# Optimization experiments

Measured on AMD Instinct MI355X. Metric: run time of the kernel, lower is better.

The kernel has to match this reference:

```python
import jax, jax.numpy as jnp
import numpy as np

N, CX, CS, H = 2048, 768, 384, 16
D = CX // H  # 48


def _ln(t, eps=1e-5):
    mu = jnp.mean(t, axis=-1, keepdims=True)
    var = jnp.mean(jnp.square(t - mu), axis=-1, keepdims=True)
    return (t - mu) * jax.lax.rsqrt(var + eps)


def setup_inputs() -> dict:
    key = jax.random.key(0)
    ks = jax.random.split(key, 16)
    s = 0.02
    return {
        "x": jax.random.normal(ks[0], (N, CX), jnp.float32),
        "mask": jax.random.randint(ks[1], (N,), 0, 2, jnp.int32),
        "pair_logits": jax.random.normal(ks[2], (H, N, N), jnp.float32),
        "single_cond": jax.random.normal(ks[3], (N, CS), jnp.float32),
        # AdaptiveLayerNorm params (single_cond LN has weight, no bias)
        "ln_sc_w": jnp.ones((CS,), jnp.float32),
        "sc_scale_w": s * jax.random.normal(ks[4], (CS, CX), jnp.float32),
        "sc_scale_b": jnp.zeros((CX,), jnp.float32),
        "sc_bias_w": s * jax.random.normal(ks[5], (CS, CX), jnp.float32),
        # q/k/v/gating projections (stored as (in, out); y = x @ W)
        "q_w": s * jax.random.normal(ks[6], (CX, CX), jnp.float32),
        "q_b": jnp.zeros((CX,), jnp.float32),
        "k_w": s * jax.random.normal(ks[7], (CX, CX), jnp.float32),
        "v_w": s * jax.random.normal(ks[8], (CX, CX), jnp.float32),
        "gate_w": s * jax.random.normal(ks[9], (CX, CX), jnp.float32),
        # AdaLNZero params
        "out_w": s * jax.random.normal(ks[10], (CX, CX), jnp.float32),
        "azc_w": s * jax.random.normal(ks[11], (CS, CX), jnp.float32),
        "azc_b": jnp.zeros((CX,), jnp.float32),
    }


def reference(x, mask, pair_logits, single_cond, ln_sc_w, sc_scale_w, sc_scale_b,
              sc_bias_w, q_w, q_b, k_w, v_w, gate_w, out_w, azc_w, azc_b):
    # AdaptiveLayerNorm (use_single_cond=True)
    xn = _ln(x)                              # (N, CX), no affine
    sc = _ln(single_cond) * ln_sc_w          # (N, CS), weight only
    xa = jax.nn.sigmoid(sc @ sc_scale_w + sc_scale_b) * xn + sc @ sc_bias_w

    # QKV projections, split into heads: (N, H, D)
    q = (xa @ q_w + q_b).reshape(N, H, D)
    k = (xa @ k_w).reshape(N, H, D)
    v = (xa @ v_w).reshape(N, H, D)

    # Attention with per-head additive pair bias and key mask
    logits = jnp.einsum("qhd,khd->hqk", q * (D ** -0.5), k) + pair_logits
    logits = jnp.where(mask.astype(bool)[None, None, :], logits, -1e9)
    w = jax.nn.softmax(logits, axis=-1)      # (H, N, N)
    wa = jnp.einsum("hqk,khd->qhd", w, v).reshape(N, CX)

    # Gating, then AdaLNZero output
    wa = wa * jax.nn.sigmoid(xa @ gate_w)
    out = (wa @ out_w) * jax.nn.sigmoid(sc @ azc_w + azc_b)
    return out
```

## Files before the change

kernel.cpp:

```cpp
#include <hip/hip_runtime.h>
#include <math.h>

#define NN 2048
#define CXX 768
#define CSS 384
#define HH 16
#define DHH 48
#define KSPLIT 2

typedef short bf16x8 __attribute__((ext_vector_type(8)));
typedef float f32x4 __attribute__((ext_vector_type(4)));

#define MFMA16(a,b,c) __builtin_amdgcn_mfma_f32_16x16x32_bf16(a,b,c,0,0,0)

__device__ __forceinline__ unsigned short f2bf(float f){
  unsigned u = __float_as_uint(f);
  u += 0x7FFFu + ((u >> 16) & 1u);
  return (unsigned short)(u >> 16);
}
__device__ __forceinline__ float bf2f(unsigned short u){
  return __uint_as_float(((unsigned)u) << 16);
}
__device__ __forceinline__ void async_copy16(const void* g, void* l){
  __builtin_amdgcn_global_load_lds((const __attribute__((address_space(1))) void*)g,
                                   (__attribute__((address_space(3))) void*)l, 16, 0, 0);
}

__device__ inline float waveReduceSum(float v){
  #pragma unroll
  for(int o=32;o>0;o>>=1) v += __shfl_xor(v,o);
  return v;
}

__global__ __launch_bounds__(256) void transpose_all(
    const float* __restrict__ s0, const float* __restrict__ s1, const float* __restrict__ s2,
    const float* __restrict__ s3, const float* __restrict__ s4, const float* __restrict__ s5,
    const float* __restrict__ s6, const float* __restrict__ s7,
    unsigned short* __restrict__ d_scale, unsigned short* __restrict__ d_bias,
    unsigned short* __restrict__ d_azc, unsigned short* __restrict__ d_qkvg,
    unsigned short* __restrict__ d_out){
  int z = blockIdx.z;
  const float* W; unsigned short* Wt; int K;
  switch(z){
    case 0: W=s0; Wt=d_scale; K=384; break;
    case 1: W=s1; Wt=d_bias;  K=384; break;
    case 2: W=s2; Wt=d_azc;   K=384; break;
    case 3: W=s3; Wt=d_qkvg + 0*589824; K=768; break;
    case 4: W=s4; Wt=d_qkvg + 1*589824; K=768; break;
    case 5: W=s5; Wt=d_qkvg + 2*589824; K=768; break;
    case 6: W=s6; Wt=d_qkvg + 3*589824; K=768; break;
    default: W=s7; Wt=d_out; K=768; break;
  }
  int n0 = blockIdx.x*32, k0 = blockIdx.y*32;
  if(k0 >= K) return;
  __shared__ unsigned short t[32][33];
  int c = threadIdx.x & 31, r = threadIdx.x >> 5;
  #pragma unroll
  for(int i=0;i<32;i+=8){
    float v = W[(size_t)(k0 + r + i)*CXX + n0 + c];
    t[c][r+i] = f2bf(v);
  }
  __syncthreads();
  #pragma unroll
  for(int i=0;i<32;i+=8){
    Wt[(size_t)(n0 + r + i)*K + k0 + c] = t[r+i][c];
  }
}

__global__ __launch_bounds__(384) void ln_fused(const float* __restrict__ x,
    const float* __restrict__ scin, const float* __restrict__ w,
    float* __restrict__ xn, unsigned short* __restrict__ scb){
  int row = blockIdx.x;
  int t = threadIdx.x;
  int wid = t>>6, lane = t&63;
  __shared__ float red[6];
  float a0 = x[(size_t)row*CXX + t];
  float a1 = x[(size_t)row*CXX + 384 + t];
  float s = waveReduceSum(a0+a1);
  if(lane==0) red[wid]=s;
  __syncthreads();
  float mu = (red[0]+red[1]+red[2]+red[3]+red[4]+red[5]) * (1.0f/CXX);
  float d0=a0-mu, d1=a1-mu;
  float q = waveReduceSum(d0*d0+d1*d1);
  __syncthreads();
  if(lane==0) red[wid]=q;
  __syncthreads();
  float var = (red[0]+red[1]+red[2]+red[3]+red[4]+red[5]) * (1.0f/CXX);
  float r = rsqrtf(var + 1e-5f);
  xn[(size_t)row*CXX + t] = d0*r;
  xn[(size_t)row*CXX + 384 + t] = d1*r;
  float b = scin[(size_t)row*CSS + t];
  float s2 = waveReduceSum(b);
  __syncthreads();
  if(lane==0) red[wid]=s2;
  __syncthreads();
  float mu2 = (red[0]+red[1]+red[2]+red[3]+red[4]+red[5]) * (1.0f/CSS);
  float d2 = b - mu2;
  float q2 = waveReduceSum(d2*d2);
  __syncthreads();
  if(lane==0) red[wid]=q2;
  __syncthreads();
  float var2 = (red[0]+red[1]+red[2]+red[3]+red[4]+red[5]) * (1.0f/CSS);
  float r2 = rsqrtf(var2 + 1e-5f);
  scb[(size_t)row*CSS + t] = f2bf(d2*r2*w[t]);
}

__global__ __launch_bounds__(256) void gemm_qkvg(const unsigned short* __restrict__ A,
    const unsigned short* __restrict__ Bt, const float* __restrict__ bias,
    unsigned short* __restrict__ C){
  __shared__ unsigned short As[128*32];
  __shared__ unsigned short Bs[128*32];
  const int tid = threadIdx.x;
  const int w = tid>>6, lane = tid&63;
  const int ln15 = lane&15, hi = lane>>4;
  const int wm = w&1, wn = w>>1;
  const int m0 = blockIdx.y*128, n0 = blockIdx.x*128;
  const int lrow = lane>>2, lk = (lane&3)*8;
  const int K = 768, NC = 3072;

  f32x4 z = {0.f,0.f,0.f,0.f};
  f32x4 acc[4][4];
  #pragma unroll
  for(int i=0;i<4;i++)
    #pragma unroll
    for(int j=0;j<4;j++) acc[i][j] = z;

  for(int k0=0;k0<K;k0+=32){
    const unsigned short* ga = A + (size_t)(m0 + w*32 + lrow)*K + k0 + lk;
    const unsigned short* gb = Bt + (size_t)(n0 + w*32 + lrow)*K + k0 + lk;
    async_copy16(ga,          &As[w*1024]);
    async_copy16(ga + 16*K,   &As[w*1024 + 512]);
    async_copy16(gb,          &Bs[w*1024]);
    async_copy16(gb + 16*K,   &Bs[w*1024 + 512]);
    __syncthreads();
    bf16x8 af[4], bfr[4];
    #pragma unroll
    for(int i=0;i<4;i++) af[i]  = *(const bf16x8*)&As[(wm*64 + i*16 + ln15)*32 + hi*8];
    #pragma unroll
    for(int j=0;j<4;j++) bfr[j] = *(const bf16x8*)&Bs[(wn*64 + j*16 + ln15)*32 + hi*8];
    #pragma unroll
    for(int i=0;i<4;i++)
      #pragma unroll
      for(int j=0;j<4;j++)
        acc[i][j] = MFMA16(af[i], bfr[j], acc[i][j]);
    __syncthreads();
  }

  #pragma unroll
  for(int i=0;i<4;i++)
    #pragma unroll
    for(int j=0;j<4;j++)
      #pragma unroll
      for(int r=0;r<4;r++){
        int gm = m0 + wm*64 + i*16 + hi*4 + r;
        int gn = n0 + wn*64 + j*16 + ln15;
        float v = acc[i][j][r];
        if(gn < 768) v += bias[gn];
        if(gn >= 2304) v = 1.0f/(1.0f + __expf(-v));
        C[(size_t)gm*NC + gn] = f2bf(v);
      }
}

__global__ __launch_bounds__(256) void adaln3(const unsigned short* __restrict__ A,
    const unsigned short* __restrict__ B1, const unsigned short* __restrict__ B2,
    const unsigned short* __restrict__ B3, const float* __restrict__ bs,
    const float* __restrict__ zb, const float* __restrict__ xn,
    unsigned short* __restrict__ xa, float* __restrict__ azc){
  __shared__ unsigned short As[64*32];
  __shared__ unsigned short Bs1[64*32];
  __shared__ unsigned short Bs2[64*32];
  __shared__ unsigned short Bs3[64*32];
  const int tid = threadIdx.x;
  const int w = tid>>6, lane = tid&63;
  const int ln15 = lane&15, hi = lane>>4;
  const int wm = w&1, wn = w>>1;
  const int m0 = blockIdx.y*64, n0 = blockIdx.x*64;
  const int lrow = tid>>2, lk = (tid&3)*8;
  const int K = CSS;

  f32x4 z = {0.f,0.f,0.f,0.f};
  f32x4 acc1[2][2], acc2[2][2], acc3[2][2];
  #pragma unroll
  for(int i=0;i<2;i++)
    #pragma unroll
    for(int j=0;j<2;j++){ acc1[i][j]=z; acc2[i][j]=z; acc3[i][j]=z; }

  for(int k0=0;k0<K;k0+=32){
    async_copy16(A  + (size_t)(m0+lrow)*K + k0 + lk, &As [w*512]);
    async_copy16(B1 + (size_t)(n0+lrow)*K + k0 + lk, &Bs1[w*512]);
    async_copy16(B2 + (size_t)(n0+lrow)*K + k0 + lk, &Bs2[w*512]);
    async_copy16(B3 + (size_t)(n0+lrow)*K + k0 + lk, &Bs3[w*512]);
    __syncthreads();
    bf16x8 af[2], b1f[2], b2f[2], b3f[2];
    #pragma unroll
    for(int i=0;i<2;i++) af[i]  = *(const bf16x8*)&As[(wm*32 + i*16 + ln15)*32 + hi*8];
    #pragma unroll
    for(int j=0;j<2;j++){
      b1f[j] = *(const bf16x8*)&Bs1[(wn*32 + j*16 + ln15)*32 + hi*8];
      b2f[j] = *(const bf16x8*)&Bs2[(wn*32 + j*16 + ln15)*32 + hi*8];
      b3f[j] = *(const bf16x8*)&Bs3[(wn*32 + j*16 + ln15)*32 + hi*8];
    }
    #pragma unroll
    for(int i=0;i<2;i++)
      #pragma unroll
      for(int j=0;j<2;j++){
        acc1[i][j] = MFMA16(af[i], b1f[j], acc1[i][j]);
        acc2[i][j] = MFMA16(af[i], b2f[j], acc2[i][j]);
        acc3[i][j] = MFMA16(af[i], b3f[j], acc3[i][j]);
      }
    __syncthreads();
  }

  #pragma unroll
  for(int i=0;i<2;i++)
    #pragma unroll
    for(int j=0;j<2;j++)
      #pragma unroll
      for(int r=0;r<4;r++){
        int gm = m0 + wm*32 + i*16 + hi*4 + r;
        int gn = n0 + wn*32 + j*16 + ln15;
        float g = 1.0f/(1.0f + __expf(-(acc1[i][j][r] + bs[gn])));
        float v = g * xn[(size_t)gm*CXX + gn] + acc2[i][j][r];
        xa[(size_t)gm*CXX + gn] = f2bf(v);
        azc[(size_t)gm*CXX + gn] = 1.0f/(1.0f + __expf(-(acc3[i][j][r] + zb[gn])));
      }
}

__global__ __launch_bounds__(256) void gemm_out(const unsigned short* __restrict__ A,
    const unsigned short* __restrict__ Bt, const float* __restrict__ mul,
    float* __restrict__ C){
  __shared__ unsigned short As[64*32];
  __shared__ unsigned short Bs[64*32];
  const int tid = threadIdx.x;
  const int w = tid>>6, lane = tid&63;
  const int ln15 = lane&15, hi = lane>>4;
  const int wm = w&1, wn = w>>1;
  const int m0 = blockIdx.y*64, n0 = blockIdx.x*64;
  const int lrow = tid>>2, lk = (tid&3)*8;
  const int K = 768;

  f32x4 z = {0.f,0.f,0.f,0.f};
  f32x4 acc[2][2];
  #pragma unroll
  for(int i=0;i<2;i++)
    #pragma unroll
    for(int j=0;j<2;j++) acc[i][j]=z;

  for(int k0=0;k0<K;k0+=32){
    async_copy16(A  + (size_t)(m0+lrow)*K + k0 + lk, &As[w*512]);
    async_copy16(Bt + (size_t)(n0+lrow)*K + k0 + lk, &Bs[w*512]);
    __syncthreads();
    bf16x8 af[2], bfr[2];
    #pragma unroll
    for(int i=0;i<2;i++) af[i]  = *(const bf16x8*)&As[(wm*32 + i*16 + ln15)*32 + hi*8];
    #pragma unroll
    for(int j=0;j<2;j++) bfr[j] = *(const bf16x8*)&Bs[(wn*32 + j*16 + ln15)*32 + hi*8];
    #pragma unroll
    for(int i=0;i<2;i++)
      #pragma unroll
      for(int j=0;j<2;j++)
        acc[i][j] = MFMA16(af[i], bfr[j], acc[i][j]);
    __syncthreads();
  }

  #pragma unroll
  for(int i=0;i<2;i++)
    #pragma unroll
    for(int j=0;j<2;j++)
      #pragma unroll
      for(int r=0;r<4;r++){
        int gm = m0 + wm*32 + i*16 + hi*4 + r;
        int gn = n0 + wn*32 + j*16 + ln15;
        C[(size_t)gm*CXX + gn] = acc[i][j][r] * mul[(size_t)gm*CXX + gn];
      }
}

__global__ __launch_bounds__(256) void attn_mfma(const unsigned short* __restrict__ qkvg,
    const float* __restrict__ pair, const int* __restrict__ mask,
    float* __restrict__ po, float* __restrict__ pm, float* __restrict__ pl){
  const int h = blockIdx.y;
  const int q0 = blockIdx.x*64;
  const int kz = blockIdx.z;
  const int kbase = kz*(NN/KSPLIT);
  const int NT = (NN/KSPLIT)/64;
  const int tid = threadIdx.x;
  const int w = tid>>6, lane = tid&63;
  const int ln15 = lane&15, hi = lane>>4;

  __shared__ unsigned short QPs[64*72];
  __shared__ unsigned short Ks[64*72];
  __shared__ unsigned short VsT[48*72];

  for(int idx=tid; idx<64*16; idx+=256){
    int row = idx>>4, d = 48 + (idx&15);
    QPs[row*72 + d] = 0;
    Ks[row*72 + d] = 0;
  }
  for(int idx=tid; idx<64*12; idx+=256){
    int qr = idx&63, d0 = (idx>>6)*4;
    ushort4 v = *(const ushort4*)&qkvg[(size_t)(q0+qr)*3072 + h*DHH + d0];
    *(ushort4*)&QPs[qr*72 + d0] = v;
  }
  __syncthreads();

  bf16x8 aq0 = *(const bf16x8*)&QPs[(w*16+ln15)*72 + hi*8];
  bf16x8 aq1 = *(const bf16x8*)&QPs[(w*16+ln15)*72 + 32 + hi*8];
  unsigned short* Ps = &QPs[w*16*72];

  f32x4 z = {0.f,0.f,0.f,0.f};
  f32x4 oacc[3] = {z,z,z};
  float mold[4] = {-1e30f,-1e30f,-1e30f,-1e30f};
  float l[4] = {0.f,0.f,0.f,0.f};
  const float scale = 0.14433756729740643f;
  const int qrb = w*16 + hi*4;

  ushort4 kreg[3], vreg[3];
  int mreg[4];
  float preg[4][4];
  {
    #pragma unroll
    for(int it=0;it<3;it++){
      int idx = tid + it*256;
      int key = idx&63, d0 = (idx>>6)*4;
      kreg[it] = *(const ushort4*)&qkvg[(size_t)(kbase+key)*3072 +  768 + h*DHH + d0];
      vreg[it] = *(const ushort4*)&qkvg[(size_t)(kbase+key)*3072 + 1536 + h*DHH + d0];
    }
    #pragma unroll
    for(int jt=0;jt<4;jt++) mreg[jt] = mask[kbase + jt*16 + ln15];
    const float* pb = pair + ((size_t)h*NN + (size_t)(q0+qrb))*NN + kbase + ln15;
    #pragma unroll
    for(int r=0;r<4;r++)
      #pragma unroll
      for(int jt=0;jt<4;jt++)
        preg[jt][r] = pb[(size_t)r*NN + jt*16];
  }

  for(int kt=0; kt<NT; ++kt){
    __syncthreads();
    #pragma unroll
    for(int it=0;it<3;it++){
      int idx = tid + it*256;
      int key = idx&63, d0 = (idx>>6)*4;
      ushort4 kv = kreg[it];
      *(ushort4*)&Ks[key*72 + d0] = kv;
      ushort4 vv = vreg[it];
      VsT[(d0+0)*72 + key] = vv.x;
      VsT[(d0+1)*72 + key] = vv.y;
      VsT[(d0+2)*72 + key] = vv.z;
      VsT[(d0+3)*72 + key] = vv.w;
    }
    __syncthreads();

    float pc[4][4]; int mc[4];
    #pragma unroll
    for(int jt=0;jt<4;jt++){
      mc[jt] = mreg[jt];
      #pragma unroll
      for(int r=0;r<4;r++) pc[jt][r] = preg[jt][r];
    }
    {
      int k0n = (kt < NT-1) ? kbase + (kt+1)*64 : kbase;
      #pragma unroll
      for(int it=0;it<3;it++){
        int idx = tid + it*256;
        int key = idx&63, d0 = (idx>>6)*4;
        kreg[it] = *(const ushort4*)&qkvg[(size_t)(k0n+key)*3072 +  768 + h*DHH + d0];
        vreg[it] = *(const ushort4*)&qkvg[(size_t)(k0n+key)*3072 + 1536 + h*DHH + d0];
      }
      #pragma unroll
      for(int jt=0;jt<4;jt++) mreg[jt] = mask[k0n + jt*16 + ln15];
      const float* pb = pair + ((size_t)h*NN + (size_t)(q0+qrb))*NN + k0n + ln15;
      #pragma unroll
      for(int r=0;r<4;r++)
        #pragma unroll
        for(int jt=0;jt<4;jt++)
          preg[jt][r] = pb[(size_t)r*NN + jt*16];
    }

    f32x4 sreg[4];
    __builtin_amdgcn_s_setprio(1);
    #pragma unroll
    for(int jt=0;jt<4;jt++){
      bf16x8 bk0 = *(const bf16x8*)&Ks[(jt*16+ln15)*72 + hi*8];
      bf16x8 bk1 = *(const bf16x8*)&Ks[(jt*16+ln15)*72 + 32 + hi*8];
      f32x4 s = z;
      s = MFMA16(aq0, bk0, s);
      s = MFMA16(aq1, bk1, s);
      sreg[jt] = s;
    }
    __builtin_amdgcn_s_setprio(0);

    float sv[4][4];
    #pragma unroll
    for(int jt=0;jt<4;jt++)
      #pragma unroll
      for(int r=0;r<4;r++)
        sv[jt][r] = mc[jt] ? sreg[jt][r]*scale + pc[jt][r] : -1e9f;

    float mr[4], al[4], rs[4];
    #pragma unroll
    for(int r=0;r<4;r++)
      mr[r] = fmaxf(fmaxf(sv[0][r],sv[1][r]), fmaxf(sv[2][r],sv[3][r]));
    #pragma unroll
    for(int o=1;o<16;o<<=1)
      #pragma unroll
      for(int r=0;r<4;r++) mr[r] = fmaxf(mr[r], __shfl_xor(mr[r],o));
    #pragma unroll
    for(int r=0;r<4;r++){
      float mn = fmaxf(mold[r], mr[r]);
      al[r] = __expf(mold[r] - mn);
      mold[r] = mn;
    }
    float pv[4][4];
    #pragma unroll
    for(int jt=0;jt<4;jt++)
      #pragma unroll
      for(int r=0;r<4;r++)
        pv[jt][r] = __expf(sv[jt][r] - mold[r]);
    #pragma unroll
    for(int r=0;r<4;r++) rs[r] = pv[0][r]+pv[1][r]+pv[2][r]+pv[3][r];
    #pragma unroll
    for(int o=1;o<16;o<<=1)
      #pragma unroll
      for(int r=0;r<4;r++) rs[r] += __shfl_xor(rs[r],o);
    #pragma unroll
    for(int r=0;r<4;r++) l[r] = l[r]*al[r] + rs[r];

    #pragma unroll
    for(int jt=0;jt<4;jt++)
      #pragma unroll
      for(int r=0;r<4;r++)
        Ps[(hi*4+r)*72 + jt*16 + ln15] = f2bf(pv[jt][r]);
    __asm__ volatile("s_waitcnt lgkmcnt(0)" ::: "memory");

    #pragma unroll
    for(int dt=0;dt<3;dt++)
      #pragma unroll
      for(int r=0;r<4;r++) oacc[dt][r] *= al[r];

    bf16x8 ap0 = *(const bf16x8*)&Ps[ln15*72 + hi*8];
    bf16x8 ap1 = *(const bf16x8*)&Ps[ln15*72 + 32 + hi*8];
    __builtin_amdgcn_s_setprio(1);
    #pragma unroll
    for(int dt=0;dt<3;dt++){
      bf16x8 bv0 = *(const bf16x8*)&VsT[(dt*16+ln15)*72 + hi*8];
      bf16x8 bv1 = *(const bf16x8*)&VsT[(dt*16+ln15)*72 + 32 + hi*8];
      oacc[dt] = MFMA16(ap0, bv0, oacc[dt]);
      oacc[dt] = MFMA16(ap1, bv1, oacc[dt]);
    }
    __builtin_amdgcn_s_setprio(0);
  }

  #pragma unroll
  for(int r=0;r<4;r++){
    int qrow = q0 + qrb + r;
    size_t rowi = (size_t)(kz*HH + h)*NN + qrow;
    #pragma unroll
    for(int dt=0;dt<3;dt++)
      po[rowi*DHH + dt*16 + ln15] = oacc[dt][r];
    if(ln15==0){
      pm[rowi] = mold[r];
      pl[rowi] = l[r];
    }
  }
}

__global__ __launch_bounds__(256) void attn_combine(const float* __restrict__ po,
    const float* __restrict__ pm, const float* __restrict__ pl,
    const unsigned short* __restrict__ qkvg, unsigned short* __restrict__ wag){
  const int row = blockIdx.x*4 + (threadIdx.x>>6);
  const int lane = threadIdx.x & 63;
  #pragma unroll
  for(int i=0;i<12;i++){
    int c = lane + i*64;
    int hh = c / DHH, d = c - hh*DHH;
    size_t r0 = (size_t)hh*NN + row;
    size_t r1 = (size_t)(HH + hh)*NN + row;
    float m0 = pm[r0], m1 = pm[r1];
    float M = fmaxf(m0, m1);
    float e0 = __expf(m0 - M), e1 = __expf(m1 - M);
    float L = pl[r0]*e0 + pl[r1]*e1;
    float v = (po[r0*DHH + d]*e0 + po[r1*DHH + d]*e1) / L;
    float g = bf2f(qkvg[(size_t)row*3072 + 2304 + c]);
    wag[(size_t)row*CXX + c] = f2bf(v * g);
  }
}

extern "C" void kernel_launch(void* const* d_in, const int* in_sizes, int n_in,
                              void* d_out, int out_size, void* d_ws, size_t ws_size,
                              hipStream_t stream) {
  const float* x           = (const float*)d_in[0];
  const int*   mask        = (const int*)  d_in[1];
  const float* pair        = (const float*)d_in[2];
  const float* single_cond = (const float*)d_in[3];
  const float* ln_sc_w     = (const float*)d_in[4];
  const float* sc_scale_w  = (const float*)d_in[5];
  const float* sc_scale_b  = (const float*)d_in[6];
  const float* sc_bias_w   = (const float*)d_in[7];
  const float* q_w         = (const float*)d_in[8];
  const float* q_b         = (const float*)d_in[9];
  const float* k_w         = (const float*)d_in[10];
  const float* v_w         = (const float*)d_in[11];
  const float* gate_w      = (const float*)d_in[12];
  const float* out_w       = (const float*)d_in[13];
  const float* azc_w       = (const float*)d_in[14];
  const float* azc_b       = (const float*)d_in[15];
  float* out = (float*)d_out;

  unsigned short* p = (unsigned short*)d_ws;
  unsigned short* Wt_scale = p;  p += 768*384;
  unsigned short* Wt_bias  = p;  p += 768*384;
  unsigned short* Wt_azc   = p;  p += 768*384;
  unsigned short* Wt_out   = p;  p += 768*768;
  unsigned short* Wt_qkvg  = p;  p += (size_t)3072*768;
  unsigned short* scb      = p;  p += 2048*384;
  unsigned short* xa       = p;  p += 2048*768;
  unsigned short* qkvg     = p;  p += (size_t)2048*3072;
  unsigned short* wag      = p;  p += 2048*768;
  float* fp = (float*)p;
  float* xn  = fp; fp += (size_t)2048*768;
  float* azc = fp; fp += (size_t)2048*768;
  float* po  = fp; fp += (size_t)KSPLIT*HH*NN*DHH;
  float* pm  = fp; fp += (size_t)KSPLIT*HH*NN;
  float* pl  = fp;

  transpose_all<<<dim3(24,24,8), 256, 0, stream>>>(
      sc_scale_w, sc_bias_w, azc_w, q_w, k_w, v_w, gate_w, out_w,
      Wt_scale, Wt_bias, Wt_azc, Wt_qkvg, Wt_out);

  ln_fused<<<NN, 384, 0, stream>>>(x, single_cond, ln_sc_w, xn, scb);

  adaln3<<<dim3(12,32), 256, 0, stream>>>(scb, Wt_scale, Wt_bias, Wt_azc,
                                          sc_scale_b, azc_b, xn, xa, azc);

  gemm_qkvg<<<dim3(24,16), 256, 0, stream>>>(xa, Wt_qkvg, q_b, qkvg);

  attn_mfma<<<dim3(32,16,KSPLIT), 256, 0, stream>>>(qkvg, pair, mask, po, pm, pl);

  attn_combine<<<512, 256, 0, stream>>>(po, pm, pl, qkvg, wag);

  gemm_out<<<dim3(12,32), 256, 0, stream>>>(wag, Wt_out, azc, out);
}
```

Measured before the change: 556.7 us.

## Load attention K/V fragments straight from global with a transposed V buffer

The QKV GEMM epilogue now writes V transposed into a separate buffer (head-dim major), so V fragments can be read in MFMA operand layout. The attention kernel drops LDS staging of Q, K and V and their block-wide barriers. Each wave loads its K and V fragments directly from global memory into registers, double-buffered across an unroll-by-two tile loop. This removes LDS transposes and __syncthreads per tile. In exchange the four waves redundantly fetch the same K/V through cache, and register pressure rises.

```diff
diff --git a/kernel.cpp b/kernel.cpp
--- a/kernel.cpp
+++ b/kernel.cpp
@@ -107,7 +107,7 @@
 
 __global__ __launch_bounds__(256) void gemm_qkvg(const unsigned short* __restrict__ A,
     const unsigned short* __restrict__ Bt, const float* __restrict__ bias,
-    unsigned short* __restrict__ C){
+    unsigned short* __restrict__ C, unsigned short* __restrict__ vt){
   __shared__ unsigned short As[128*32];
   __shared__ unsigned short Bs[128*32];
   const int tid = threadIdx.x;
@@ -149,16 +149,26 @@
   #pragma unroll
   for(int i=0;i<4;i++)
     #pragma unroll
-    for(int j=0;j<4;j++)
-      #pragma unroll
-      for(int r=0;r<4;r++){
-        int gm = m0 + wm*64 + i*16 + hi*4 + r;
-        int gn = n0 + wn*64 + j*16 + ln15;
-        float v = acc[i][j][r];
-        if(gn < 768) v += bias[gn];
-        if(gn >= 2304) v = 1.0f/(1.0f + __expf(-v));
-        C[(size_t)gm*NC + gn] = f2bf(v);
+    for(int j=0;j<4;j++){
+      int gm0 = m0 + wm*64 + i*16 + hi*4;
+      int gn  = n0 + wn*64 + j*16 + ln15;
+      if(gn >= 1536 && gn < 2304){
+        ushort4 v4;
+        v4.x = f2bf(acc[i][j][0]);
+        v4.y = f2bf(acc[i][j][1]);
+        v4.z = f2bf(acc[i][j][2]);
+        v4.w = f2bf(acc[i][j][3]);
+        *(ushort4*)&vt[(size_t)(gn - 1536)*NN + gm0] = v4;
+      } else {
+        #pragma unroll
+        for(int r=0;r<4;r++){
+          float v = acc[i][j][r];
+          if(gn < 768) v += bias[gn];
+          if(gn >= 2304) v = 1.0f/(1.0f + __expf(-v));
+          C[(size_t)(gm0+r)*NC + gn] = f2bf(v);
+        }
       }
+    }
 }
 
 __global__ __launch_bounds__(256) void adaln3(const unsigned short* __restrict__ A,
@@ -275,9 +285,103 @@
       }
 }
 
+
+#define LOAD_TILE(B, KOFF) do{                                                     \
+    int kk_ = (KOFF);                                                              \
+    _Pragma("unroll")                                                              \
+    for(int jt=0;jt<4;jt++){                                                       \
+      const unsigned short* kp_ = qkvg + (size_t)(kk_ + jt*16 + ln15)*3072 + 768 + h*DHH + hi*8; \
+      kf0[B][jt] = *(const bf16x8*)kp_;                                            \
+      kf1[B][jt] = *(const bf16x8*)(kp_ + 32);                                     \
+    }                                                                              \
+    _Pragma("unroll")                                                              \
+    for(int jt=0;jt<4;jt++) mkr[B][jt] = mask[kk_ + jt*16 + ln15];                 \
+    const float* pb_ = pair + ((size_t)h*NN + (size_t)(q0+qrb))*NN + kk_ + ln15;   \
+    _Pragma("unroll")                                                              \
+    for(int r=0;r<4;r++)                                                           \
+      _Pragma("unroll")                                                            \
+      for(int jt=0;jt<4;jt++)                                                      \
+        pfr[B][jt][r] = pb_[(size_t)r*NN + jt*16];                                 \
+  }while(0)
+
+#define ATTN_TILE(B, NB, KCUR, KNXT) do{                                           \
+    bf16x8 vf0[3], vf1[3];                                                         \
+    _Pragma("unroll")                                                              \
+    for(int dt=0;dt<3;dt++){                                                       \
+      const unsigned short* vp_ = vt + (size_t)(h*DHH + dt*16 + ln15)*NN + (KCUR) + hi*8; \
+      vf0[dt] = *(const bf16x8*)vp_;                                               \
+      vf1[dt] = *(const bf16x8*)(vp_ + 32);                                        \
+    }                                                                              \
+    f32x4 sreg[4];                                                                 \
+    __builtin_amdgcn_s_setprio(1);                                                 \
+    _Pragma("unroll")                                                              \
+    for(int jt=0;jt<4;jt++){                                                       \
+      f32x4 s_ = z;                                                                \
+      s_ = MFMA16(aq0, kf0[B][jt], s_);                                            \
+      s_ = MFMA16(aq1, kf1[B][jt], s_);                                            \
+      sreg[jt] = s_;                                                               \
+    }                                                                              \
+    __builtin_amdgcn_s_setprio(0);                                                 \
+    LOAD_TILE(NB, KNXT);                                                           \
+    float sv[4][4];                                                                \
+    _Pragma("unroll")                                                              \
+    for(int jt=0;jt<4;jt++)                                                        \
+      _Pragma("unroll")                                                            \
+      for(int r=0;r<4;r++)                                                         \
+        sv[jt][r] = mkr[B][jt] ? sreg[jt][r]*scale + pfr[B][jt][r] : -1e9f;        \
+    float mrow[4], al[4], rs[4];                                                   \
+    _Pragma("unroll")                                                              \
+    for(int r=0;r<4;r++)                                                           \
+      mrow[r] = fmaxf(fmaxf(sv[0][r],sv[1][r]), fmaxf(sv[2][r],sv[3][r]));         \
+    _Pragma("unroll")                                                              \
+    for(int o=1;o<16;o<<=1)                                                        \
+      _Pragma("unroll")                                                            \
+      for(int r=0;r<4;r++) mrow[r] = fmaxf(mrow[r], __shfl_xor(mrow[r],o));        \
+    _Pragma("unroll")                                                              \
+    for(int r=0;r<4;r++){                                                          \
+      float mn_ = fmaxf(mold[r], mrow[r]);                                         \
+      al[r] = __expf(mold[r] - mn_);                                               \
+      mold[r] = mn_;                                                               \
+    }                                                                              \
+    float pv[4][4];                                                                \
+    _Pragma("unroll")                                                              \
+    for(int jt=0;jt<4;jt++)                                                        \
+      _Pragma("unroll")                                                            \
+      for(int r=0;r<4;r++)                                                         \
+        pv[jt][r] = __expf(sv[jt][r] - mold[r]);                                   \
+    _Pragma("unroll")                                                              \
+    for(int r=0;r<4;r++) rs[r] = pv[0][r]+pv[1][r]+pv[2][r]+pv[3][r];              \
+    _Pragma("unroll")                                                              \
+    for(int o=1;o<16;o<<=1)                                                        \
+      _Pragma("unroll")                                                            \
+      for(int r=0;r<4;r++) rs[r] += __shfl_xor(rs[r],o);                           \
+    _Pragma("unroll")                                                              \
+    for(int r=0;r<4;r++) l[r] = l[r]*al[r] + rs[r];                                \
+    _Pragma("unroll")                                                              \
+    for(int jt=0;jt<4;jt++)                                                        \
+      _Pragma("unroll")                                                            \
+      for(int r=0;r<4;r++)                                                         \
+        Ps[w][(hi*4+r)*72 + jt*16 + ln15] = f2bf(pv[jt][r]);                       \
+    __asm__ volatile("s_waitcnt lgkmcnt(0)" ::: "memory");                         \
+    _Pragma("unroll")                                                              \
+    for(int dt=0;dt<3;dt++)                                                        \
+      _Pragma("unroll")                                                            \
+      for(int r=0;r<4;r++) oacc[dt][r] *= al[r];                                   \
+    bf16x8 ap0 = *(const bf16x8*)&Ps[w][ln15*72 + hi*8];                           \
+    bf16x8 ap1 = *(const bf16x8*)&Ps[w][ln15*72 + 32 + hi*8];                      \
+    __builtin_amdgcn_s_setprio(1);                                                 \
+    _Pragma("unroll")                                                              \
+    for(int dt=0;dt<3;dt++){                                                       \
+      oacc[dt] = MFMA16(ap0, vf0[dt], oacc[dt]);                                   \
+      oacc[dt] = MFMA16(ap1, vf1[dt], oacc[dt]);                                   \
+    }                                                                              \
+    __builtin_amdgcn_s_setprio(0);                                                 \
+  }while(0)
+
 __global__ __launch_bounds__(256) void attn_mfma(const unsigned short* __restrict__ qkvg,
-    const float* __restrict__ pair, const int* __restrict__ mask,
-    float* __restrict__ po, float* __restrict__ pm, float* __restrict__ pl){
+    const unsigned short* __restrict__ vt, const float* __restrict__ pair,
+    const int* __restrict__ mask, float* __restrict__ po, float* __restrict__ pm,
+    float* __restrict__ pl){
   const int h = blockIdx.y;
   const int q0 = blockIdx.x*64;
   const int kz = blockIdx.z;
@@ -286,169 +390,37 @@
   const int tid = threadIdx.x;
   const int w = tid>>6, lane = tid&63;
   const int ln15 = lane&15, hi = lane>>4;
-
-  __shared__ unsigned short QPs[64*72];
-  __shared__ unsigned short Ks[64*72];
-  __shared__ unsigned short VsT[48*72];
-
-  for(int idx=tid; idx<64*16; idx+=256){
-    int row = idx>>4, d = 48 + (idx&15);
-    QPs[row*72 + d] = 0;
-    Ks[row*72 + d] = 0;
-  }
-  for(int idx=tid; idx<64*12; idx+=256){
-    int qr = idx&63, d0 = (idx>>6)*4;
-    ushort4 v = *(const ushort4*)&qkvg[(size_t)(q0+qr)*3072 + h*DHH + d0];
-    *(ushort4*)&QPs[qr*72 + d0] = v;
-  }
-  __syncthreads();
-
-  bf16x8 aq0 = *(const bf16x8*)&QPs[(w*16+ln15)*72 + hi*8];
-  bf16x8 aq1 = *(const bf16x8*)&QPs[(w*16+ln15)*72 + 32 + hi*8];
-  unsigned short* Ps = &QPs[w*16*72];
-
+  const int qrb = w*16 + hi*4;
+
+  __shared__ unsigned short Ps[4][16*72];
+
+  const float scale = 0.14433756729740643f;
   f32x4 z = {0.f,0.f,0.f,0.f};
+
+  const unsigned short* qp = qkvg + (size_t)(q0 + w*16 + ln15)*3072 + h*DHH + hi*8;
+  bf16x8 aq0 = *(const bf16x8*)qp;
+  bf16x8 aq1 = *(const bf16x8*)(qp + 32);
+  {
+    bf16x8 z8 = {0,0,0,0,0,0,0,0};
+    if(hi >= 2) aq1 = z8;
+  }
+
   f32x4 oacc[3] = {z,z,z};
   float mold[4] = {-1e30f,-1e30f,-1e30f,-1e30f};
   float l[4] = {0.f,0.f,0.f,0.f};
-  const float scale = 0.14433756729740643f;
-  const int qrb = w*16 + hi*4;
-
-  ushort4 kreg[3], vreg[3];
-  int mreg[4];
-  float preg[4][4];
-  {
-    #pragma unroll
-    for(int it=0;it<3;it++){
-      int idx = tid + it*256;
-      int key = idx&63, d0 = (idx>>6)*4;
-      kreg[it] = *(const ushort4*)&qkvg[(size_t)(kbase+key)*3072 +  768 + h*DHH + d0];
-      vreg[it] = *(const ushort4*)&qkvg[(size_t)(kbase+key)*3072 + 1536 + h*DHH + d0];
-    }
-    #pragma unroll
-    for(int jt=0;jt<4;jt++) mreg[jt] = mask[kbase + jt*16 + ln15];
-    const float* pb = pair + ((size_t)h*NN + (size_t)(q0+qrb))*NN + kbase + ln15;
-    #pragma unroll
-    for(int r=0;r<4;r++)
-      #pragma unroll
-      for(int jt=0;jt<4;jt++)
-        preg[jt][r] = pb[(size_t)r*NN + jt*16];
-  }
-
-  for(int kt=0; kt<NT; ++kt){
-    __syncthreads();
-    #pragma unroll
-    for(int it=0;it<3;it++){
-      int idx = tid + it*256;
-      int key = idx&63, d0 = (idx>>6)*4;
-      ushort4 kv = kreg[it];
-      *(ushort4*)&Ks[key*72 + d0] = kv;
-      ushort4 vv = vreg[it];
-      VsT[(d0+0)*72 + key] = vv.x;
-      VsT[(d0+1)*72 + key] = vv.y;
-      VsT[(d0+2)*72 + key] = vv.z;
-      VsT[(d0+3)*72 + key] = vv.w;
-    }
-    __syncthreads();
-
-    float pc[4][4]; int mc[4];
-    #pragma unroll
-    for(int jt=0;jt<4;jt++){
-      mc[jt] = mreg[jt];
-      #pragma unroll
-      for(int r=0;r<4;r++) pc[jt][r] = preg[jt][r];
-    }
-    {
-      int k0n = (kt < NT-1) ? kbase + (kt+1)*64 : kbase;
-      #pragma unroll
-      for(int it=0;it<3;it++){
-        int idx = tid + it*256;
-        int key = idx&63, d0 = (idx>>6)*4;
-        kreg[it] = *(const ushort4*)&qkvg[(size_t)(k0n+key)*3072 +  768 + h*DHH + d0];
-        vreg[it] = *(const ushort4*)&qkvg[(size_t)(k0n+key)*3072 + 1536 + h*DHH + d0];
-      }
-      #pragma unroll
-      for(int jt=0;jt<4;jt++) mreg[jt] = mask[k0n + jt*16 + ln15];
-      const float* pb = pair + ((size_t)h*NN + (size_t)(q0+qrb))*NN + k0n + ln15;
-      #pragma unroll
-      for(int r=0;r<4;r++)
-        #pragma unroll
-        for(int jt=0;jt<4;jt++)
-          preg[jt][r] = pb[(size_t)r*NN + jt*16];
-    }
-
-    f32x4 sreg[4];
-    __builtin_amdgcn_s_setprio(1);
-    #pragma unroll
-    for(int jt=0;jt<4;jt++){
-      bf16x8 bk0 = *(const bf16x8*)&Ks[(jt*16+ln15)*72 + hi*8];
-      bf16x8 bk1 = *(const bf16x8*)&Ks[(jt*16+ln15)*72 + 32 + hi*8];
-      f32x4 s = z;
-      s = MFMA16(aq0, bk0, s);
-      s = MFMA16(aq1, bk1, s);
-      sreg[jt] = s;
-    }
-    __builtin_amdgcn_s_setprio(0);
-
-    float sv[4][4];
-    #pragma unroll
-    for(int jt=0;jt<4;jt++)
-      #pragma unroll
-      for(int r=0;r<4;r++)
-        sv[jt][r] = mc[jt] ? sreg[jt][r]*scale + pc[jt][r] : -1e9f;
-
-    float mr[4], al[4], rs[4];
-    #pragma unroll
-    for(int r=0;r<4;r++)
-      mr[r] = fmaxf(fmaxf(sv[0][r],sv[1][r]), fmaxf(sv[2][r],sv[3][r]));
-    #pragma unroll
-    for(int o=1;o<16;o<<=1)
-      #pragma unroll
-      for(int r=0;r<4;r++) mr[r] = fmaxf(mr[r], __shfl_xor(mr[r],o));
-    #pragma unroll
-    for(int r=0;r<4;r++){
-      float mn = fmaxf(mold[r], mr[r]);
-      al[r] = __expf(mold[r] - mn);
-      mold[r] = mn;
-    }
-    float pv[4][4];
-    #pragma unroll
-    for(int jt=0;jt<4;jt++)
-      #pragma unroll
-      for(int r=0;r<4;r++)
-        pv[jt][r] = __expf(sv[jt][r] - mold[r]);
-    #pragma unroll
-    for(int r=0;r<4;r++) rs[r] = pv[0][r]+pv[1][r]+pv[2][r]+pv[3][r];
-    #pragma unroll
-    for(int o=1;o<16;o<<=1)
-      #pragma unroll
-      for(int r=0;r<4;r++) rs[r] += __shfl_xor(rs[r],o);
-    #pragma unroll
-    for(int r=0;r<4;r++) l[r] = l[r]*al[r] + rs[r];
-
-    #pragma unroll
-    for(int jt=0;jt<4;jt++)
-      #pragma unroll
-      for(int r=0;r<4;r++)
-        Ps[(hi*4+r)*72 + jt*16 + ln15] = f2bf(pv[jt][r]);
-    __asm__ volatile("s_waitcnt lgkmcnt(0)" ::: "memory");
-
-    #pragma unroll
-    for(int dt=0;dt<3;dt++)
-      #pragma unroll
-      for(int r=0;r<4;r++) oacc[dt][r] *= al[r];
-
-    bf16x8 ap0 = *(const bf16x8*)&Ps[ln15*72 + hi*8];
-    bf16x8 ap1 = *(const bf16x8*)&Ps[ln15*72 + 32 + hi*8];
-    __builtin_amdgcn_s_setprio(1);
-    #pragma unroll
-    for(int dt=0;dt<3;dt++){
-      bf16x8 bv0 = *(const bf16x8*)&VsT[(dt*16+ln15)*72 + hi*8];
-      bf16x8 bv1 = *(const bf16x8*)&VsT[(dt*16+ln15)*72 + 32 + hi*8];
-      oacc[dt] = MFMA16(ap0, bv0, oacc[dt]);
-      oacc[dt] = MFMA16(ap1, bv1, oacc[dt]);
-    }
-    __builtin_amdgcn_s_setprio(0);
+
+  bf16x8 kf0[2][4], kf1[2][4];
+  float  pfr[2][4][4];
+  int    mkr[2][4];
+
+  LOAD_TILE(0, kbase);
+
+  for(int t=0; t<NT/2; ++t){
+    int k0c = kbase + (2*t)*64;
+    int k1c = kbase + (2*t+1)*64;
+    int k2n = (2*t+2 < NT) ? kbase + (2*t+2)*64 : kbase;
+    ATTN_TILE(0, 1, k0c, k1c);
+    ATTN_TILE(1, 0, k1c, k2n);
   }
 
   #pragma unroll
@@ -517,6 +489,7 @@
   unsigned short* xa       = p;  p += 2048*768;
   unsigned short* qkvg     = p;  p += (size_t)2048*3072;
   unsigned short* wag      = p;  p += 2048*768;
+  unsigned short* vt       = p;  p += (size_t)768*2048;
   float* fp = (float*)p;
   float* xn  = fp; fp += (size_t)2048*768;
   float* azc = fp; fp += (size_t)2048*768;
@@ -533,9 +506,9 @@
   adaln3<<<dim3(12,32), 256, 0, stream>>>(scb, Wt_scale, Wt_bias, Wt_azc,
                                           sc_scale_b, azc_b, xn, xa, azc);
 
-  gemm_qkvg<<<dim3(24,16), 256, 0, stream>>>(xa, Wt_qkvg, q_b, qkvg);
-
-  attn_mfma<<<dim3(32,16,KSPLIT), 256, 0, stream>>>(qkvg, pair, mask, po, pm, pl);
+  gemm_qkvg<<<dim3(24,16), 256, 0, stream>>>(xa, Wt_qkvg, q_b, qkvg, vt);
+
+  attn_mfma<<<dim3(32,16,KSPLIT), 256, 0, stream>>>(qkvg, vt, pair, mask, po, pm, pl);
 
   attn_combine<<<512, 256, 0, stream>>>(po, pm, pl, qkvg, wag);
 
```

Result: faster. 539.3 us (-3.1%).
